# Performance work log

Measured on AMD Instinct MI355X. Metric: run time of the kernel, lower is better.

Reference implementation:

```python
import jax, jax.numpy as jnp
import numpy as np

B, C, H, W = 256, 3, 224, 224
CROP = 190


def _persp_coeffs(end):
    # torchvision _get_perspective_coeffs: solve for (a..h) with
    # (a*ex+b*ey+c)/(g*ex+h*ey+1)=sx, (d*ex+e*ey+f)/(g*ex+h*ey+1)=sy
    start = jnp.array([[0., 0.], [223., 0.], [223., 223.], [0., 223.]], jnp.float32)
    ex, ey = end[:, 0], end[:, 1]
    sx, sy = start[:, 0], start[:, 1]
    o = jnp.ones(4, jnp.float32); z = jnp.zeros(4, jnp.float32)
    r1 = jnp.stack([ex, ey, o, z, z, z, -sx * ex, -sx * ey], axis=-1)
    r2 = jnp.stack([z, z, z, ex, ey, o, -sy * ex, -sy * ey], axis=-1)
    A = jnp.concatenate([r1, r2], axis=0)  # [8,8]
    b = jnp.concatenate([sx, sy], axis=0)
    return jnp.linalg.solve(A, b)


def _bilinear(img, sx, sy):
    # img [C,H,W]; sx,sy [H,W] source index coords; zero padding outside.
    Hh, Ww = img.shape[-2], img.shape[-1]
    x0 = jnp.floor(sx); y0 = jnp.floor(sy)
    wx = sx - x0; wy = sy - y0
    x0i = x0.astype(jnp.int32); y0i = y0.astype(jnp.int32)

    def tap(yi, xi, w):
        valid = ((xi >= 0) & (xi < Ww) & (yi >= 0) & (yi < Hh)).astype(img.dtype)
        v = img[:, jnp.clip(yi, 0, Hh - 1), jnp.clip(xi, 0, Ww - 1)]
        return v * (w * valid)[None]

    return (tap(y0i, x0i, (1 - wx) * (1 - wy)) + tap(y0i, x0i + 1, wx * (1 - wy))
            + tap(y0i + 1, x0i, (1 - wx) * wy) + tap(y0i + 1, x0i + 1, wx * wy))


def _augment(x, noise, brightness, flip_mask, ep_raw, angles, crop_ij):
    Bb, Cc, Hh, Ww = x.shape
    # random hflip
    x = jnp.where(flip_mask[:, None, None, None] > 0, x[..., ::-1], x)
    # gaussian noise (std 0.625) and brightness in [0.85, 1.15]
    x = x + 0.625 * noise
    x = x * (0.85 + 0.30 * brightness)[:, None, None, None]
    # batched perspective warp (bilinear, zero fill)
    offs = jnp.array([[0., 0.], [195., 0.], [195., 195.], [0., 195.]], jnp.float32)
    end = ep_raw.astype(jnp.float32) + offs  # [B,4,2] endpoints
    coeffs = jax.vmap(_persp_coeffs)(end)    # [B,8]
    Xg, Yg = jnp.meshgrid(jnp.arange(Ww, dtype=jnp.float32) + 0.5,
                          jnp.arange(Hh, dtype=jnp.float32) + 0.5, indexing='xy')
    a, b, c, d, e, f, g, h = [coeffs[:, i][:, None, None] for i in range(8)]
    den = g * Xg + h * Yg + 1.0
    sx = (a * Xg + b * Yg + c) / den - 0.5  # half-pixel centers, align_corners=False
    sy = (d * Xg + e * Yg + f) / den - 0.5
    x = jax.vmap(_bilinear)(x, sx, sy)
    # batched rotation about image center (bilinear, zero fill)
    th = (angles.astype(jnp.float32) - 16.0) * (jnp.pi / 180.0)
    cos = jnp.cos(th)[:, None, None]; sin = jnp.sin(th)[:, None, None]
    cx = (Ww - 1) / 2.0; cy = (Hh - 1) / 2.0
    dx = (Xg - 0.5) - cx; dy = (Yg - 0.5) - cy
    rx = cos * dx + sin * dy + cx
    ry = -sin * dx + cos * dy + cy
    x = jax.vmap(_bilinear)(x, rx, ry)
    # per-sample 190x190 crop
    x = jax.vmap(lambda img, ij: jax.lax.dynamic_slice(
        img, (0, ij[0], ij[1]), (Cc, CROP, CROP)))(x, crop_ij)
    # bicubic resize back to 224x224
    x = jax.image.resize(x, (Bb, Cc, Hh, Ww), method='bicubic')
    return x


def setup_inputs() -> dict:
    key = jax.random.key(0)
    ks = jax.random.split(key, 7)
    return {
        'x': jax.random.uniform(ks[0], (B, C, H, W), dtype=jnp.float32),
        'noise': jax.random.normal(ks[1], (B, C, H, W), dtype=jnp.float32),
        'brightness': jax.random.uniform(ks[2], (B,), dtype=jnp.float32),
        'flip_mask': jax.random.randint(ks[3], (B,), 0, 2, dtype=jnp.int32),
        'ep_raw': jax.random.randint(ks[4], (B, 4, 2), 0, 29, dtype=jnp.int32),
        'angles': jax.random.randint(ks[5], (B,), 0, 33, dtype=jnp.int32),
        'crop_ij': jax.random.randint(ks[6], (B, 2), 0, 35, dtype=jnp.int32),
    }


def reference(x, noise, brightness, flip_mask, ep_raw, angles, crop_ij):
    return _augment(x, noise, brightness, flip_mask, ep_raw, angles, crop_ij)
```

## Files before the change

### kernel.cpp

```cpp
#include <hip/hip_runtime.h>
#include <math.h>

#define Bn 256
#define Cn 3
#define Hn 224
#define Wn 224
#define CROPD 190

static constexpr long long NTOT = (long long)Bn * Cn * Hn * Wn;
static constexpr int PLANE = Hn * Wn;

#define TILE 32
#define TSTR 68
#define PH 48
#define PSTR 52
#define RSTR 40

#define NWG (768 * 49)
#define CHUNK (NWG / 8)

__device__ int    g_i0[Wn];
__device__ float4 g_wt[Wn];

__device__ __forceinline__ float keys_cubic(float x) {
    if (x < 1.f) return ((1.5f * x - 2.5f) * x) * x + 1.f;
    if (x < 2.f) return ((-0.5f * x + 2.5f) * x - 4.f) * x + 2.f;
    return 0.f;
}
__device__ __forceinline__ float rflf(float v) {
    return __int_as_float(__builtin_amdgcn_readfirstlane(__float_as_int(v)));
}
__device__ __forceinline__ int rfli(int v) { return __builtin_amdgcn_readfirstlane(v); }
__device__ __forceinline__ int swz_block(int bid) {
    return (bid & 7) * CHUNK + (bid >> 3);
}

__global__ void params_kernel(const int* __restrict__ ep_raw,
                              const int* __restrict__ angles,
                              const float* __restrict__ brightness,
                              const int* __restrict__ flip_mask,
                              float* __restrict__ params) {
    int b = threadIdx.x;

    if (b < Wn) {
        float sf = ((float)b + 0.5f) * ((float)CROPD / (float)Wn) - 0.5f;
        int i0 = (int)floorf(sf);
        float w[4]; float s = 0.f;
#pragma unroll
        for (int k = 0; k < 4; k++) {
            int idx = i0 - 1 + k;
            float wk = (idx >= 0 && idx < CROPD) ? keys_cubic(fabsf(sf - (float)idx)) : 0.f;
            w[k] = wk; s += wk;
        }
        float inv = 1.f / s;
        g_i0[b] = i0;
        g_wt[b] = make_float4(w[0] * inv, w[1] * inv, w[2] * inv, w[3] * inv);
    }

    if (b >= Bn) return;

    const double offx[4] = {0.0, 195.0, 195.0, 0.0};
    const double offy[4] = {0.0, 0.0, 195.0, 195.0};
    const double sxc[4]  = {0.0, 223.0, 223.0, 0.0};
    const double syc[4]  = {0.0, 0.0, 223.0, 223.0};
    double M[8][9];
    for (int i = 0; i < 4; i++) {
        double ex = (double)ep_raw[b * 8 + i * 2 + 0] + offx[i];
        double ey = (double)ep_raw[b * 8 + i * 2 + 1] + offy[i];
        double sx = sxc[i], sy = syc[i];
        M[i][0] = ex; M[i][1] = ey; M[i][2] = 1.0;
        M[i][3] = 0.0; M[i][4] = 0.0; M[i][5] = 0.0;
        M[i][6] = -sx * ex; M[i][7] = -sx * ey; M[i][8] = sx;
        M[i + 4][0] = 0.0; M[i + 4][1] = 0.0; M[i + 4][2] = 0.0;
        M[i + 4][3] = ex; M[i + 4][4] = ey; M[i + 4][5] = 1.0;
        M[i + 4][6] = -sy * ex; M[i + 4][7] = -sy * ey; M[i + 4][8] = sy;
    }
    for (int k = 0; k < 8; k++) {
        int piv = k; double best = fabs(M[k][k]);
        for (int r = k + 1; r < 8; r++) {
            double v = fabs(M[r][k]);
            if (v > best) { best = v; piv = r; }
        }
        if (piv != k)
            for (int j = 0; j < 9; j++) { double tt = M[k][j]; M[k][j] = M[piv][j]; M[piv][j] = tt; }
        double inv = 1.0 / M[k][k];
        for (int r = k + 1; r < 8; r++) {
            double f = M[r][k] * inv;
            M[r][k] = 0.0;
            for (int j = k + 1; j < 9; j++) M[r][j] -= f * M[k][j];
        }
    }
    double sol[8];
    for (int k = 7; k >= 0; k--) {
        double s = M[k][8];
        for (int j = k + 1; j < 8; j++) s -= M[k][j] * sol[j];
        sol[k] = s / M[k][k];
    }
    float* p = params + b * 12;
    for (int j = 0; j < 8; j++) p[j] = (float)sol[j];
    double th = ((double)angles[b] - 16.0) * (M_PI / 180.0);
    p[8]  = (float)cos(th);
    p[9]  = (float)sin(th);
    p[10] = 0.85f + 0.3f * brightness[b];
    p[11] = (flip_mask[b] > 0) ? 1.0f : 0.0f;
}

__global__ void meta_kernel(const float* __restrict__ params,
                            const int* __restrict__ crop_ij,
                            int4* __restrict__ pmeta,
                            int4* __restrict__ rmeta) {
    int bt = blockIdx.x * 256 + threadIdx.x;
    int b = bt / 49, t = bt % 49;
    int ty = (t / 7) * TILE, tx = (t % 7) * TILE;
    const float* prm = params + b * 12;

    {
        float a0 = prm[0], a1 = prm[1], a2 = prm[2];
        float a3 = prm[3], a4 = prm[4], a5 = prm[5];
        float g = prm[6], h = prm[7];
        float minsx = 1e30f, maxsx = -1e30f, minsy = 1e30f, maxsy = -1e30f;
#pragma unroll
        for (int cy = 0; cy < 2; cy++) {
#pragma unroll
            for (int cxr = 0; cxr < 2; cxr++) {
                float Xg = (float)tx + (cxr ? 31.5f : 0.5f);
                float Yg = (float)ty + (cy ? 31.5f : 0.5f);
                float rden = 1.0f / (g * Xg + h * Yg + 1.0f);
                float sx = (a0 * Xg + a1 * Yg + a2) * rden - 0.5f;
                float sy = (a3 * Xg + a4 * Yg + a5) * rden - 0.5f;
                minsx = fminf(minsx, sx); maxsx = fmaxf(maxsx, sx);
                minsy = fminf(minsy, sy); maxsy = fmaxf(maxsy, sy);
            }
        }
        int x0b = min(max((int)floorf(minsx) - 1, 0), Wn - 1);
        int x1b = min(max((int)floorf(maxsx) + 2, 0), Wn - 1);
        int y0b = min(max((int)floorf(minsy) - 1, 0), Hn - 1);
        int y1b = min(max((int)floorf(maxsy) + 2, 0), Hn - 1);
        x0b &= ~3;
        int bw = x1b - x0b + 1, bh = y1b - y0b + 1;
        int inter = (minsx >= 0.5f && maxsx <= 222.0f &&
                     minsy >= 0.5f && maxsy <= 222.0f) ? 1 : 0;
        pmeta[bt] = make_int4(x0b, y0b, bw | (inter << 16), bh);
    }

    {
        float cs = prm[8], sn = prm[9];
        int ci = crop_ij[b * 2 + 0], cj = crop_ij[b * 2 + 1];
        int iymin = max(g_i0[ty] - 1, 0);
        int iymax = min(g_i0[ty + 31] + 2, CROPD - 1);
        int jmin = max(g_i0[tx] - 1, 0);
        int jmax = min(g_i0[tx + 31] + 2, CROPD - 1);
        int ry0 = iymin + ci, ry1 = iymax + ci;
        int rx0 = jmin + cj, rx1 = jmax + cj;
        const float cxc = (Wn - 1) * 0.5f;
        float minrx = 1e30f, maxrx = -1e30f, minry = 1e30f, maxry = -1e30f;
#pragma unroll
        for (int cy = 0; cy < 2; cy++) {
#pragma unroll
            for (int cxr = 0; cxr < 2; cxr++) {
                float dx = (float)(cxr ? rx1 : rx0) - cxc;
                float dy = (float)(cy ? ry1 : ry0) - cxc;
                float rx = cs * dx + sn * dy + cxc;
                float ry = -sn * dx + cs * dy + cxc;
                minrx = fminf(minrx, rx); maxrx = fmaxf(maxrx, rx);
                minry = fminf(minry, ry); maxry = fmaxf(maxry, ry);
            }
        }
        int x0b = min(max((int)floorf(minrx) - 1, 0), Wn - 1);
        int x1b = min(max((int)floorf(maxrx) + 2, 0), Wn - 1);
        int y0b = min(max((int)floorf(minry) - 1, 0), Hn - 1);
        int y1b = min(max((int)floorf(maxry) + 2, 0), Hn - 1);
        x0b &= ~3;
        int bw = x1b - x0b + 1, bh = y1b - y0b + 1;
        int inter = (minrx >= 0.5f && maxrx <= 222.0f &&
                     minry >= 0.5f && maxry <= 222.0f) ? 1 : 0;
        rmeta[bt] = make_int4(x0b, y0b, bw | (inter << 16), bh);
    }
}

__global__ __launch_bounds__(256) void persp_kernel(const float* __restrict__ xin,
                                                    const float* __restrict__ noise,
                                                    const float* __restrict__ params,
                                                    const int4* __restrict__ pmeta,
                                                    float* __restrict__ outP) {
    __shared__ __align__(16) float lds[64 * TSTR];
    int bi = swz_block(blockIdx.x);
    int p = bi / 49;
    int t = bi % 49;
    int ty = (t / 7) * TILE;
    int tx = (t % 7) * TILE;
    int b = p / Cn;
    int4 m = pmeta[b * 49 + t];
    int x0b = m.x, y0b = m.y;
    int bw = m.z & 0xffff;
    bool interior = (m.z >> 16) != 0;
    int bh = m.w;
    int y1b = y0b + bh - 1;
    bool use_lds = (bw <= 64) && (bh <= 64);

    const float* prm = params + b * 12;
    float a0 = rflf(prm[0]), a1 = rflf(prm[1]), a2 = rflf(prm[2]);
    float a3 = rflf(prm[3]), a4 = rflf(prm[4]), a5 = rflf(prm[5]);
    float g = rflf(prm[6]), h = rflf(prm[7]), bf = rflf(prm[10]);
    bool flip = rflf(prm[11]) > 0.5f;

    const size_t base = (size_t)p * PLANE;
    const float* xb = xin + base;
    const float* nb = noise + base;
    int tid = threadIdx.x;

    if (use_lds) {
        int bwq = (bw + 3) >> 2;
        int sh = (bwq <= 8) ? 3 : 4;
        int c4 = tid & ((1 << sh) - 1);
        int r0 = tid >> sh;
        int rstep = 256 >> sh;
        bool cok = c4 < bwq;
        for (int yy = y0b + r0; yy <= y1b; yy += rstep) {
            if (cok) {
                int xl = min(x0b + c4 * 4, Wn - 4);
                float4 nv = *reinterpret_cast<const float4*>(&nb[yy * Wn + xl]);
                float4 xv;
                if (flip) {
                    float4 xr = *reinterpret_cast<const float4*>(&xb[yy * Wn + (Wn - 4 - xl)]);
                    xv = make_float4(xr.w, xr.z, xr.y, xr.x);
                } else {
                    xv = *reinterpret_cast<const float4*>(&xb[yy * Wn + xl]);
                }
                float4 f = make_float4((xv.x + 0.625f * nv.x) * bf,
                                       (xv.y + 0.625f * nv.y) * bf,
                                       (xv.z + 0.625f * nv.z) * bf,
                                       (xv.w + 0.625f * nv.w) * bf);
                *reinterpret_cast<float4*>(&lds[(yy - y0b) * TSTR + (xl - x0b)]) = f;
            }
        }
        __syncthreads();
    }

    int r = tid >> 3;
    int cg = tid & 7;
    int oy = ty + r, ox0 = tx + cg * 4;
    float Yg = (float)oy + 0.5f;
    float Xg0 = (float)ox0 + 0.5f;
    float nx = a0 * Xg0 + a1 * Yg + a2;
    float ny = a3 * Xg0 + a4 * Yg + a5;
    float dn = g * Xg0 + h * Yg + 1.0f;
    float racc[4];
    if (use_lds && interior) {
#pragma unroll
        for (int o = 0; o < 4; o++) {
            float rden = __builtin_amdgcn_rcpf(dn);
            float sx = nx * rden - 0.5f;
            float sy = ny * rden - 0.5f;
            float fx0 = floorf(sx), fy0 = floorf(sy);
            float wx = sx - fx0, wy = sy - fy0;
            const float* q = &lds[((int)fy0 - y0b) * TSTR + ((int)fx0 - x0b)];
            float top = q[0] + wx * (q[1] - q[0]);
            float bot = q[TSTR] + wx * (q[TSTR + 1] - q[TSTR]);
            racc[o] = top + wy * (bot - top);
            nx += a0; ny += a3; dn += g;
        }
    } else {
#pragma unroll
        for (int o = 0; o < 4; o++) {
            float rden = __builtin_amdgcn_rcpf(dn);
            float sx = nx * rden - 0.5f;
            float sy = ny * rden - 0.5f;
            float fx0 = floorf(sx), fy0 = floorf(sy);
            float wx = sx - fx0, wy = sy - fy0;
            int x0 = (int)fx0, y0 = (int)fy0;
            float acc = 0.f;
#pragma unroll
            for (int dy = 0; dy < 2; dy++) {
                int yy = y0 + dy;
                float wyv = dy ? wy : 1.f - wy;
                bool yv = (unsigned)yy < (unsigned)Hn;
                int yc = min(max(yy, 0), Hn - 1);
#pragma unroll
                for (int dx = 0; dx < 2; dx++) {
                    int xx = x0 + dx;
                    float wxv = dx ? wx : 1.f - wx;
                    bool v = yv && ((unsigned)xx < (unsigned)Wn);
                    int xc = min(max(xx, 0), Wn - 1);
                    float wgt = v ? wxv * wyv : 0.f;
                    float val;
                    if (use_lds) {
                        val = lds[(yc - y0b) * TSTR + (xc - x0b)];
                    } else {
                        int xsrc = flip ? (Wn - 1 - xc) : xc;
                        val = (xb[yc * Wn + xsrc] + 0.625f * nb[yc * Wn + xc]) * bf;
                    }
                    acc += val * wgt;
                }
            }
            racc[o] = acc;
            nx += a0; ny += a3; dn += g;
        }
    }
    *reinterpret_cast<float4*>(outP + base + (size_t)oy * Wn + ox0) =
        make_float4(racc[0], racc[1], racc[2], racc[3]);
}

__global__ __launch_bounds__(256) void rotresize_kernel(const float* __restrict__ P,
                                                        const float* __restrict__ params,
                                                        const int* __restrict__ crop_ij,
                                                        const int4* __restrict__ rmeta,
                                                        float* __restrict__ out) {
    __shared__ __align__(16) float Plds[PH * PSTR];
    __shared__ __align__(16) float Rlds[32 * RSTR];
    __shared__ __align__(16) float Tlds[32 * RSTR];
    int bi = swz_block(blockIdx.x);
    int p = bi / 49;
    int t = bi % 49;
    int ty = (t / 7) * TILE;
    int tx = (t % 7) * TILE;
    int b = p / Cn;
    int4 m = rmeta[b * 49 + t];
    int x0b = m.x, y0b = m.y;
    int bw = m.z & 0xffff;
    bool interior = (m.z >> 16) != 0;
    int bh = m.w;
    int y1b = y0b + bh - 1;
    bool use_lds = (bw <= PH) && (bh <= PH);

    const float* prm = params + b * 12;
    float cs = rflf(prm[8]), sn = rflf(prm[9]);
    int ci = rfli(crop_ij[b * 2 + 0]);
    int cj = rfli(crop_ij[b * 2 + 1]);
    int iymin = max(g_i0[ty] - 1, 0);
    int nTy = min(g_i0[ty + 31] + 2, CROPD - 1) - iymin + 1;
    int jmin = max(g_i0[tx] - 1, 0);
    int nRx = min(g_i0[tx + 31] + 2, CROPD - 1) - jmin + 1;
    int rx0 = jmin + cj, ry0 = iymin + ci;
    const float cxc = (Wn - 1) * 0.5f;

    const float* Pb = P + (size_t)p * PLANE;
    int tid = threadIdx.x;

    if (use_lds) {
        int bwq = (bw + 3) >> 2;
        int sh = (bwq <= 8) ? 3 : 4;
        int c4 = tid & ((1 << sh) - 1);
        int r0 = tid >> sh;
        int rstep = 256 >> sh;
        bool cok = c4 < bwq;
        for (int yy = y0b + r0; yy <= y1b; yy += rstep) {
            if (cok) {
                int xl = min(x0b + c4 * 4, Wn - 4);
                float4 v = *reinterpret_cast<const float4*>(&Pb[yy * Wn + xl]);
                *reinterpret_cast<float4*>(&Plds[(yy - y0b) * PSTR + (xl - x0b)]) = v;
            }
        }
        __syncthreads();
    }

    {
        int rc = tid & 31;
        int rbase = tid >> 5;
        bool cok = rc < nRx;
        float dxc = (float)(rx0 + rc) - cxc;
        float bx = cs * dxc + cxc;
        float by = -sn * dxc + cxc;
        if (use_lds && interior) {
#pragma unroll
            for (int it = 0; it < 4; it++) {
                int rr = it * 8 + rbase;
                if (rr < nTy && cok) {
                    float dyr = (float)(ry0 + rr) - cxc;
                    float srx = bx + sn * dyr;
                    float sry = by + cs * dyr;
                    float fx0 = floorf(srx), fy0 = floorf(sry);
                    float wx = srx - fx0, wy = sry - fy0;
                    const float* q = &Plds[((int)fy0 - y0b) * PSTR + ((int)fx0 - x0b)];
                    float top = q[0] + wx * (q[1] - q[0]);
                    float bot = q[PSTR] + wx * (q[PSTR + 1] - q[PSTR]);
                    Rlds[rr * RSTR + rc] = top + wy * (bot - top);
                }
            }
        } else {
#pragma unroll
            for (int it = 0; it < 4; it++) {
                int rr = it * 8 + rbase;
                if (rr < nTy && cok) {
                    float dyr = (float)(ry0 + rr) - cxc;
                    float srx = bx + sn * dyr;
                    float sry = by + cs * dyr;
                    float fx0 = floorf(srx), fy0 = floorf(sry);
                    float wx = srx - fx0, wy = sry - fy0;
                    int x0 = (int)fx0, y0 = (int)fy0;
                    float acc = 0.f;
#pragma unroll
                    for (int ddy = 0; ddy < 2; ddy++) {
                        int yy = y0 + ddy;
                        float wyv = ddy ? wy : 1.f - wy;
                        bool yv = (unsigned)yy < (unsigned)Hn;
                        int yc = min(max(yy, 0), Hn - 1);
#pragma unroll
                        for (int ddx = 0; ddx < 2; ddx++) {
                            int xx = x0 + ddx;
                            float wxv = ddx ? wx : 1.f - wx;
                            bool v = yv && ((unsigned)xx < (unsigned)Wn);
                            int xc = min(max(xx, 0), Wn - 1);
                            float wgt = v ? wxv * wyv : 0.f;
                            float val = use_lds ? Plds[(yc - y0b) * PSTR + (xc - x0b)]
                                                : Pb[yc * Wn + xc];
                            acc += val * wgt;
                        }
                    }
                    Rlds[rr * RSTR + rc] = acc;
                }
            }
        }
    }
    __syncthreads();

    {
        int oc = tid & 31;
        int rbase = tid >> 5;
        int ox = tx + oc;
        float4 w = g_wt[ox];
        int j0 = g_i0[ox];
        int jc0 = min(max(j0 - 1, 0), CROPD - 1) - jmin;
        int jc1 = min(max(j0 + 0, 0), CROPD - 1) - jmin;
        int jc2 = min(max(j0 + 1, 0), CROPD - 1) - jmin;
        int jc3 = min(max(j0 + 2, 0), CROPD - 1) - jmin;
#pragma unroll
        for (int it = 0; it < 4; it++) {
            int rr = it * 8 + rbase;
            if (rr < nTy) {
                const float* row = &Rlds[rr * RSTR];
                Tlds[rr * RSTR + oc] = w.x * row[jc0] + w.y * row[jc1] +
                                       w.z * row[jc2] + w.w * row[jc3];
            }
        }
    }
    __syncthreads();

    {
        int r = tid >> 3, cg = tid & 7;
        int oy = ty + r, ox0 = tx + cg * 4;
        float4 w = g_wt[oy];
        int i0y = g_i0[oy];
        float wk[4] = {w.x, w.y, w.z, w.w};
        float4 acc = make_float4(0.f, 0.f, 0.f, 0.f);
#pragma unroll
        for (int k = 0; k < 4; k++) {
            int iyc = min(max(i0y - 1 + k, 0), CROPD - 1) - iymin;
            float4 v = *reinterpret_cast<const float4*>(&Tlds[iyc * RSTR + cg * 4]);
            acc.x += wk[k] * v.x;
            acc.y += wk[k] * v.y;
            acc.z += wk[k] * v.z;
            acc.w += wk[k] * v.w;
        }
        *reinterpret_cast<float4*>(out + (size_t)p * PLANE + (size_t)oy * Wn + ox0) = acc;
    }
}

extern "C" void kernel_launch(void* const* d_in, const int* in_sizes, int n_in,
                              void* d_out, int out_size, void* d_ws, size_t ws_size,
                              hipStream_t stream) {
    const float* x          = (const float*)d_in[0];
    const float* noise      = (const float*)d_in[1];
    const float* brightness = (const float*)d_in[2];
    const int*   flip_mask  = (const int*)d_in[3];
    const int*   ep_raw     = (const int*)d_in[4];
    const int*   angles     = (const int*)d_in[5];
    const int*   crop_ij    = (const int*)d_in[6];
    float* out = (float*)d_out;

    float* params = (float*)d_ws;
    int4*  pmeta  = (int4*)((char*)d_ws + 16384);
    int4*  rmeta  = (int4*)((char*)d_ws + 16384 + 200704);
    float* Pbuf   = (float*)((char*)d_ws + (1 << 20));

    params_kernel<<<1, 256, 0, stream>>>(ep_raw, angles, brightness, flip_mask, params);
    meta_kernel<<<49, 256, 0, stream>>>(params, crop_ij, pmeta, rmeta);
    persp_kernel<<<NWG, 256, 0, stream>>>(x, noise, params, pmeta, Pbuf);
    rotresize_kernel<<<NWG, 256, 0, stream>>>(Pbuf, params, crop_ij, rmeta, out);
}
```

Before: 273.6 us.

## Fuse perspective warp into rotate-resize kernel, eliminating intermediate buffer

Merges the perspective kernel and the rotate/crop/resize kernel into one. Each tile now computes, in LDS, only the perspective-warped region its rotation needs, working from a staged input footprint derived by back-projecting the rotation bounding box. This removes the full-size intermediate write and re-read in global memory, plus one launch. The cost is redundant perspective computation across neighbouring tiles' overlapping halos, more LDS per block, and a slow global fallback path that recomputes the perspective per tap.

```diff
diff --git a/kernel.cpp b/kernel.cpp
--- a/kernel.cpp
+++ b/kernel.cpp
@@ -7,12 +7,12 @@
 #define Wn 224
 #define CROPD 190
 
-static constexpr long long NTOT = (long long)Bn * Cn * Hn * Wn;
 static constexpr int PLANE = Hn * Wn;
 
 #define TILE 32
-#define TSTR 68
-#define PH 48
+#define FH 72
+#define FSTR 76
+#define PHR 48
 #define PSTR 52
 #define RSTR 40
 
@@ -107,42 +107,14 @@
 
 __global__ void meta_kernel(const float* __restrict__ params,
                             const int* __restrict__ crop_ij,
-                            int4* __restrict__ pmeta,
-                            int4* __restrict__ rmeta) {
+                            int4* __restrict__ rmeta,
+                            int4* __restrict__ smeta) {
     int bt = blockIdx.x * 256 + threadIdx.x;
     int b = bt / 49, t = bt % 49;
     int ty = (t / 7) * TILE, tx = (t % 7) * TILE;
     const float* prm = params + b * 12;
 
-    {
-        float a0 = prm[0], a1 = prm[1], a2 = prm[2];
-        float a3 = prm[3], a4 = prm[4], a5 = prm[5];
-        float g = prm[6], h = prm[7];
-        float minsx = 1e30f, maxsx = -1e30f, minsy = 1e30f, maxsy = -1e30f;
-#pragma unroll
-        for (int cy = 0; cy < 2; cy++) {
-#pragma unroll
-            for (int cxr = 0; cxr < 2; cxr++) {
-                float Xg = (float)tx + (cxr ? 31.5f : 0.5f);
-                float Yg = (float)ty + (cy ? 31.5f : 0.5f);
-                float rden = 1.0f / (g * Xg + h * Yg + 1.0f);
-                float sx = (a0 * Xg + a1 * Yg + a2) * rden - 0.5f;
-                float sy = (a3 * Xg + a4 * Yg + a5) * rden - 0.5f;
-                minsx = fminf(minsx, sx); maxsx = fmaxf(maxsx, sx);
-                minsy = fminf(minsy, sy); maxsy = fmaxf(maxsy, sy);
-            }
-        }
-        int x0b = min(max((int)floorf(minsx) - 1, 0), Wn - 1);
-        int x1b = min(max((int)floorf(maxsx) + 2, 0), Wn - 1);
-        int y0b = min(max((int)floorf(minsy) - 1, 0), Hn - 1);
-        int y1b = min(max((int)floorf(maxsy) + 2, 0), Hn - 1);
-        x0b &= ~3;
-        int bw = x1b - x0b + 1, bh = y1b - y0b + 1;
-        int inter = (minsx >= 0.5f && maxsx <= 222.0f &&
-                     minsy >= 0.5f && maxsy <= 222.0f) ? 1 : 0;
-        pmeta[bt] = make_int4(x0b, y0b, bw | (inter << 16), bh);
-    }
-
+    int x0p, y0p, bwp, bhp;
     {
         float cs = prm[8], sn = prm[9];
         int ci = crop_ij[b * 2 + 0], cj = crop_ij[b * 2 + 1];
@@ -170,55 +142,144 @@
         int x1b = min(max((int)floorf(maxrx) + 2, 0), Wn - 1);
         int y0b = min(max((int)floorf(minry) - 1, 0), Hn - 1);
         int y1b = min(max((int)floorf(maxry) + 2, 0), Hn - 1);
-        x0b &= ~3;
-        int bw = x1b - x0b + 1, bh = y1b - y0b + 1;
+        x0p = x0b; y0p = y0b;
+        bwp = x1b - x0b + 1; bhp = y1b - y0b + 1;
         int inter = (minrx >= 0.5f && maxrx <= 222.0f &&
                      minry >= 0.5f && maxry <= 222.0f) ? 1 : 0;
-        rmeta[bt] = make_int4(x0b, y0b, bw | (inter << 16), bh);
-    }
-}
-
-__global__ __launch_bounds__(256) void persp_kernel(const float* __restrict__ xin,
-                                                    const float* __restrict__ noise,
-                                                    const float* __restrict__ params,
-                                                    const int4* __restrict__ pmeta,
-                                                    float* __restrict__ outP) {
-    __shared__ __align__(16) float lds[64 * TSTR];
+        rmeta[bt] = make_int4(x0b, y0b, bwp | (inter << 16), bhp);
+    }
+
+    {
+        float a0 = prm[0], a1 = prm[1], a2 = prm[2];
+        float a3 = prm[3], a4 = prm[4], a5 = prm[5];
+        float g = prm[6], h = prm[7];
+        int x1p = x0p + bwp - 1, y1p = y0p + bhp - 1;
+        float minsx = 1e30f, maxsx = -1e30f, minsy = 1e30f, maxsy = -1e30f;
+#pragma unroll
+        for (int cy = 0; cy < 2; cy++) {
+#pragma unroll
+            for (int cxr = 0; cxr < 2; cxr++) {
+                float Xg = (float)(cxr ? x1p : x0p) + 0.5f;
+                float Yg = (float)(cy ? y1p : y0p) + 0.5f;
+                float rden = 1.0f / (g * Xg + h * Yg + 1.0f);
+                float sx = (a0 * Xg + a1 * Yg + a2) * rden - 0.5f;
+                float sy = (a3 * Xg + a4 * Yg + a5) * rden - 0.5f;
+                minsx = fminf(minsx, sx); maxsx = fmaxf(maxsx, sx);
+                minsy = fminf(minsy, sy); maxsy = fmaxf(maxsy, sy);
+            }
+        }
+        int x0s = min(max((int)floorf(minsx) - 1, 0), Wn - 1);
+        int x1s = min(max((int)floorf(maxsx) + 2, 0), Wn - 1);
+        int y0s = min(max((int)floorf(minsy) - 1, 0), Hn - 1);
+        int y1s = min(max((int)floorf(maxsy) + 2, 0), Hn - 1);
+        x0s &= ~3;
+        int bws = x1s - x0s + 1, bhs = y1s - y0s + 1;
+        int inter = (minsx >= 0.5f && maxsx <= 222.0f &&
+                     minsy >= 0.5f && maxsy <= 222.0f) ? 1 : 0;
+        smeta[bt] = make_int4(x0s, y0s, bws | (inter << 16), bhs);
+    }
+}
+
+__device__ __forceinline__ float persp_at(const float* __restrict__ xb,
+                                          const float* __restrict__ nb,
+                                          bool flip, float bf,
+                                          float a0, float a1, float a2,
+                                          float a3, float a4, float a5,
+                                          float g, float h, int ixp, int iyp) {
+    float Xg = (float)ixp + 0.5f, Yg = (float)iyp + 0.5f;
+    float rden = __builtin_amdgcn_rcpf(g * Xg + h * Yg + 1.0f);
+    float sx = (a0 * Xg + a1 * Yg + a2) * rden - 0.5f;
+    float sy = (a3 * Xg + a4 * Yg + a5) * rden - 0.5f;
+    float fx0 = floorf(sx), fy0 = floorf(sy);
+    float wx = sx - fx0, wy = sy - fy0;
+    int x0 = (int)fx0, y0 = (int)fy0;
+    float acc = 0.f;
+#pragma unroll
+    for (int dy = 0; dy < 2; dy++) {
+        int yy = y0 + dy;
+        float wyv = dy ? wy : 1.f - wy;
+        bool yv = (unsigned)yy < (unsigned)Hn;
+        int yc = min(max(yy, 0), Hn - 1);
+#pragma unroll
+        for (int dx = 0; dx < 2; dx++) {
+            int xx = x0 + dx;
+            float wxv = dx ? wx : 1.f - wx;
+            bool v = yv && ((unsigned)xx < (unsigned)Wn);
+            int xc = min(max(xx, 0), Wn - 1);
+            float wgt = v ? wxv * wyv : 0.f;
+            int xs = flip ? (Wn - 1 - xc) : xc;
+            acc += (xb[yc * Wn + xs] + 0.625f * nb[yc * Wn + xc]) * bf * wgt;
+        }
+    }
+    return acc;
+}
+
+__global__ __launch_bounds__(256) void mega_kernel(const float* __restrict__ xin,
+                                                   const float* __restrict__ noise,
+                                                   const float* __restrict__ params,
+                                                   const int* __restrict__ crop_ij,
+                                                   const int4* __restrict__ rmeta,
+                                                   const int4* __restrict__ smeta,
+                                                   float* __restrict__ out) {
+    __shared__ __align__(16) float smem[FH * FSTR + PHR * PSTR];
+    float* Flds = smem;
+    float* Plds = smem + FH * FSTR;
+    float* Rlds = smem;
+    float* Tlds = smem + 32 * RSTR;
+
     int bi = swz_block(blockIdx.x);
     int p = bi / 49;
     int t = bi % 49;
     int ty = (t / 7) * TILE;
     int tx = (t % 7) * TILE;
     int b = p / Cn;
-    int4 m = pmeta[b * 49 + t];
-    int x0b = m.x, y0b = m.y;
-    int bw = m.z & 0xffff;
-    bool interior = (m.z >> 16) != 0;
-    int bh = m.w;
-    int y1b = y0b + bh - 1;
-    bool use_lds = (bw <= 64) && (bh <= 64);
+    int tid = threadIdx.x;
+
+    int4 rm = rmeta[b * 49 + t];
+    int x0p = rm.x, y0p = rm.y;
+    int bwp = rm.z & 0xffff;
+    bool interior_r = (rm.z >> 16) != 0;
+    int bhp = rm.w;
+    int4 sm = smeta[b * 49 + t];
+    int x0s = sm.x, y0s = sm.y;
+    int bws = sm.z & 0xffff;
+    bool interior_s = (sm.z >> 16) != 0;
+    int bhs = sm.w;
+    int y1s = y0s + bhs - 1;
+    bool fitF = (bws <= FH) && (bhs <= FH);
+    bool fitP = (bwp <= PHR) && (bhp <= PHR);
+    bool fast = fitF && fitP;
 
     const float* prm = params + b * 12;
     float a0 = rflf(prm[0]), a1 = rflf(prm[1]), a2 = rflf(prm[2]);
     float a3 = rflf(prm[3]), a4 = rflf(prm[4]), a5 = rflf(prm[5]);
     float g = rflf(prm[6]), h = rflf(prm[7]), bf = rflf(prm[10]);
+    float cs = rflf(prm[8]), sn = rflf(prm[9]);
     bool flip = rflf(prm[11]) > 0.5f;
+    int ci = rfli(crop_ij[b * 2 + 0]);
+    int cj = rfli(crop_ij[b * 2 + 1]);
+
+    int iymin = max(g_i0[ty] - 1, 0);
+    int nTy = min(g_i0[ty + 31] + 2, CROPD - 1) - iymin + 1;
+    int jmin = max(g_i0[tx] - 1, 0);
+    int nRx = min(g_i0[tx + 31] + 2, CROPD - 1) - jmin + 1;
+    int rx0 = jmin + cj, ry0 = iymin + ci;
+    const float cxc = (Wn - 1) * 0.5f;
 
     const size_t base = (size_t)p * PLANE;
     const float* xb = xin + base;
     const float* nb = noise + base;
-    int tid = threadIdx.x;
-
-    if (use_lds) {
-        int bwq = (bw + 3) >> 2;
-        int sh = (bwq <= 8) ? 3 : 4;
+
+    if (fast) {
+        int bwq = (bws + 3) >> 2;
+        int sh = (bwq <= 8) ? 3 : ((bwq <= 16) ? 4 : 5);
         int c4 = tid & ((1 << sh) - 1);
         int r0 = tid >> sh;
         int rstep = 256 >> sh;
         bool cok = c4 < bwq;
-        for (int yy = y0b + r0; yy <= y1b; yy += rstep) {
+        for (int yy = y0s + r0; yy <= y1s; yy += rstep) {
             if (cok) {
-                int xl = min(x0b + c4 * 4, Wn - 4);
+                int xl = min(x0s + c4 * 4, Wn - 4);
                 float4 nv = *reinterpret_cast<const float4*>(&nb[yy * Wn + xl]);
                 float4 xv;
                 if (flip) {
@@ -231,128 +292,80 @@
                                        (xv.y + 0.625f * nv.y) * bf,
                                        (xv.z + 0.625f * nv.z) * bf,
                                        (xv.w + 0.625f * nv.w) * bf);
-                *reinterpret_cast<float4*>(&lds[(yy - y0b) * TSTR + (xl - x0b)]) = f;
-            }
-        }
-        __syncthreads();
-    }
-
-    int r = tid >> 3;
-    int cg = tid & 7;
-    int oy = ty + r, ox0 = tx + cg * 4;
-    float Yg = (float)oy + 0.5f;
-    float Xg0 = (float)ox0 + 0.5f;
-    float nx = a0 * Xg0 + a1 * Yg + a2;
-    float ny = a3 * Xg0 + a4 * Yg + a5;
-    float dn = g * Xg0 + h * Yg + 1.0f;
-    float racc[4];
-    if (use_lds && interior) {
-#pragma unroll
-        for (int o = 0; o < 4; o++) {
-            float rden = __builtin_amdgcn_rcpf(dn);
-            float sx = nx * rden - 0.5f;
-            float sy = ny * rden - 0.5f;
-            float fx0 = floorf(sx), fy0 = floorf(sy);
-            float wx = sx - fx0, wy = sy - fy0;
-            const float* q = &lds[((int)fy0 - y0b) * TSTR + ((int)fx0 - x0b)];
-            float top = q[0] + wx * (q[1] - q[0]);
-            float bot = q[TSTR] + wx * (q[TSTR + 1] - q[TSTR]);
-            racc[o] = top + wy * (bot - top);
-            nx += a0; ny += a3; dn += g;
-        }
-    } else {
-#pragma unroll
-        for (int o = 0; o < 4; o++) {
-            float rden = __builtin_amdgcn_rcpf(dn);
-            float sx = nx * rden - 0.5f;
-            float sy = ny * rden - 0.5f;
-            float fx0 = floorf(sx), fy0 = floorf(sy);
-            float wx = sx - fx0, wy = sy - fy0;
-            int x0 = (int)fx0, y0 = (int)fy0;
-            float acc = 0.f;
-#pragma unroll
-            for (int dy = 0; dy < 2; dy++) {
-                int yy = y0 + dy;
-                float wyv = dy ? wy : 1.f - wy;
-                bool yv = (unsigned)yy < (unsigned)Hn;
-                int yc = min(max(yy, 0), Hn - 1);
-#pragma unroll
-                for (int dx = 0; dx < 2; dx++) {
-                    int xx = x0 + dx;
-                    float wxv = dx ? wx : 1.f - wx;
-                    bool v = yv && ((unsigned)xx < (unsigned)Wn);
-                    int xc = min(max(xx, 0), Wn - 1);
-                    float wgt = v ? wxv * wyv : 0.f;
-                    float val;
-                    if (use_lds) {
-                        val = lds[(yc - y0b) * TSTR + (xc - x0b)];
-                    } else {
-                        int xsrc = flip ? (Wn - 1 - xc) : xc;
-                        val = (xb[yc * Wn + xsrc] + 0.625f * nb[yc * Wn + xc]) * bf;
+                *reinterpret_cast<float4*>(&Flds[(yy - y0s) * FSTR + (xl - x0s)]) = f;
+            }
+        }
+    }
+    __syncthreads();
+
+    if (fast) {
+        int bwpq = (bwp + 3) >> 2;
+        int c4 = tid & 15;
+        int r0 = tid >> 4;
+        bool cok = c4 < bwpq;
+        int x1p = x0p + bwp - 1;
+        if (interior_s) {
+            for (int pr = r0; pr < bhp; pr += 16) {
+                if (!cok) continue;
+                float Yg = (float)(y0p + pr) + 0.5f;
+                float pv[4];
+#pragma unroll
+                for (int j = 0; j < 4; j++) {
+                    int px = min(x0p + c4 * 4 + j, x1p);
+                    float Xg = (float)px + 0.5f;
+                    float rden = __builtin_amdgcn_rcpf(g * Xg + h * Yg + 1.0f);
+                    float sx = (a0 * Xg + a1 * Yg + a2) * rden - 0.5f;
+                    float sy = (a3 * Xg + a4 * Yg + a5) * rden - 0.5f;
+                    float fx0 = floorf(sx), fy0 = floorf(sy);
+                    float wx = sx - fx0, wy = sy - fy0;
+                    const float* q = &Flds[((int)fy0 - y0s) * FSTR + ((int)fx0 - x0s)];
+                    float top = q[0] + wx * (q[1] - q[0]);
+                    float bot = q[FSTR] + wx * (q[FSTR + 1] - q[FSTR]);
+                    pv[j] = top + wy * (bot - top);
+                }
+                *reinterpret_cast<float4*>(&Plds[pr * PSTR + c4 * 4]) =
+                    make_float4(pv[0], pv[1], pv[2], pv[3]);
+            }
+        } else {
+            for (int pr = r0; pr < bhp; pr += 16) {
+                if (!cok) continue;
+                float Yg = (float)(y0p + pr) + 0.5f;
+                float pv[4];
+#pragma unroll
+                for (int j = 0; j < 4; j++) {
+                    int px = min(x0p + c4 * 4 + j, x1p);
+                    float Xg = (float)px + 0.5f;
+                    float rden = __builtin_amdgcn_rcpf(g * Xg + h * Yg + 1.0f);
+                    float sx = (a0 * Xg + a1 * Yg + a2) * rden - 0.5f;
+                    float sy = (a3 * Xg + a4 * Yg + a5) * rden - 0.5f;
+                    float fx0 = floorf(sx), fy0 = floorf(sy);
+                    float wx = sx - fx0, wy = sy - fy0;
+                    int x0 = (int)fx0, y0 = (int)fy0;
+                    float acc = 0.f;
+#pragma unroll
+                    for (int dy = 0; dy < 2; dy++) {
+                        int yy = y0 + dy;
+                        float wyv = dy ? wy : 1.f - wy;
+                        bool yv = (unsigned)yy < (unsigned)Hn;
+                        int yc = min(max(yy, 0), Hn - 1);
+#pragma unroll
+                        for (int dx = 0; dx < 2; dx++) {
+                            int xx = x0 + dx;
+                            float wxv = dx ? wx : 1.f - wx;
+                            bool v = yv && ((unsigned)xx < (unsigned)Wn);
+                            int xc = min(max(xx, 0), Wn - 1);
+                            float wgt = v ? wxv * wyv : 0.f;
+                            acc += Flds[(yc - y0s) * FSTR + (xc - x0s)] * wgt;
+                        }
                     }
-                    acc += val * wgt;
+                    pv[j] = acc;
                 }
-            }
-            racc[o] = acc;
-            nx += a0; ny += a3; dn += g;
-        }
-    }
-    *reinterpret_cast<float4*>(outP + base + (size_t)oy * Wn + ox0) =
-        make_float4(racc[0], racc[1], racc[2], racc[3]);
-}
-
-__global__ __launch_bounds__(256) void rotresize_kernel(const float* __restrict__ P,
-                                                        const float* __restrict__ params,
-                                                        const int* __restrict__ crop_ij,
-                                                        const int4* __restrict__ rmeta,
-                                                        float* __restrict__ out) {
-    __shared__ __align__(16) float Plds[PH * PSTR];
-    __shared__ __align__(16) float Rlds[32 * RSTR];
-    __shared__ __align__(16) float Tlds[32 * RSTR];
-    int bi = swz_block(blockIdx.x);
-    int p = bi / 49;
-    int t = bi % 49;
-    int ty = (t / 7) * TILE;
-    int tx = (t % 7) * TILE;
-    int b = p / Cn;
-    int4 m = rmeta[b * 49 + t];
-    int x0b = m.x, y0b = m.y;
-    int bw = m.z & 0xffff;
-    bool interior = (m.z >> 16) != 0;
-    int bh = m.w;
-    int y1b = y0b + bh - 1;
-    bool use_lds = (bw <= PH) && (bh <= PH);
-
-    const float* prm = params + b * 12;
-    float cs = rflf(prm[8]), sn = rflf(prm[9]);
-    int ci = rfli(crop_ij[b * 2 + 0]);
-    int cj = rfli(crop_ij[b * 2 + 1]);
-    int iymin = max(g_i0[ty] - 1, 0);
-    int nTy = min(g_i0[ty + 31] + 2, CROPD - 1) - iymin + 1;
-    int jmin = max(g_i0[tx] - 1, 0);
-    int nRx = min(g_i0[tx + 31] + 2, CROPD - 1) - jmin + 1;
-    int rx0 = jmin + cj, ry0 = iymin + ci;
-    const float cxc = (Wn - 1) * 0.5f;
-
-    const float* Pb = P + (size_t)p * PLANE;
-    int tid = threadIdx.x;
-
-    if (use_lds) {
-        int bwq = (bw + 3) >> 2;
-        int sh = (bwq <= 8) ? 3 : 4;
-        int c4 = tid & ((1 << sh) - 1);
-        int r0 = tid >> sh;
-        int rstep = 256 >> sh;
-        bool cok = c4 < bwq;
-        for (int yy = y0b + r0; yy <= y1b; yy += rstep) {
-            if (cok) {
-                int xl = min(x0b + c4 * 4, Wn - 4);
-                float4 v = *reinterpret_cast<const float4*>(&Pb[yy * Wn + xl]);
-                *reinterpret_cast<float4*>(&Plds[(yy - y0b) * PSTR + (xl - x0b)]) = v;
-            }
-        }
-        __syncthreads();
-    }
+                *reinterpret_cast<float4*>(&Plds[pr * PSTR + c4 * 4]) =
+                    make_float4(pv[0], pv[1], pv[2], pv[3]);
+            }
+        }
+    }
+    __syncthreads();
 
     {
         int rc = tid & 31;
@@ -361,7 +374,7 @@
         float dxc = (float)(rx0 + rc) - cxc;
         float bx = cs * dxc + cxc;
         float by = -sn * dxc + cxc;
-        if (use_lds && interior) {
+        if (fast && interior_r) {
 #pragma unroll
             for (int it = 0; it < 4; it++) {
                 int rr = it * 8 + rbase;
@@ -371,13 +384,13 @@
                     float sry = by + cs * dyr;
                     float fx0 = floorf(srx), fy0 = floorf(sry);
                     float wx = srx - fx0, wy = sry - fy0;
-                    const float* q = &Plds[((int)fy0 - y0b) * PSTR + ((int)fx0 - x0b)];
+                    const float* q = &Plds[((int)fy0 - y0p) * PSTR + ((int)fx0 - x0p)];
                     float top = q[0] + wx * (q[1] - q[0]);
                     float bot = q[PSTR] + wx * (q[PSTR + 1] - q[PSTR]);
                     Rlds[rr * RSTR + rc] = top + wy * (bot - top);
                 }
             }
-        } else {
+        } else if (fast) {
 #pragma unroll
             for (int it = 0; it < 4; it++) {
                 int rr = it * 8 + rbase;
@@ -402,9 +415,40 @@
                             bool v = yv && ((unsigned)xx < (unsigned)Wn);
                             int xc = min(max(xx, 0), Wn - 1);
                             float wgt = v ? wxv * wyv : 0.f;
-                            float val = use_lds ? Plds[(yc - y0b) * PSTR + (xc - x0b)]
-                                                : Pb[yc * Wn + xc];
-                            acc += val * wgt;
+                            acc += Plds[(yc - y0p) * PSTR + (xc - x0p)] * wgt;
+                        }
+                    }
+                    Rlds[rr * RSTR + rc] = acc;
+                }
+            }
+        } else {
+#pragma unroll
+            for (int it = 0; it < 4; it++) {
+                int rr = it * 8 + rbase;
+                if (rr < nTy && cok) {
+                    float dyr = (float)(ry0 + rr) - cxc;
+                    float srx = bx + sn * dyr;
+                    float sry = by + cs * dyr;
+                    float fx0 = floorf(srx), fy0 = floorf(sry);
+                    float wx = srx - fx0, wy = sry - fy0;
+                    int x0 = (int)fx0, y0 = (int)fy0;
+                    float acc = 0.f;
+#pragma unroll
+                    for (int ddy = 0; ddy < 2; ddy++) {
+                        int yy = y0 + ddy;
+                        float wyv = ddy ? wy : 1.f - wy;
+                        bool yv = (unsigned)yy < (unsigned)Hn;
+                        int yc = min(max(yy, 0), Hn - 1);
+#pragma unroll
+                        for (int ddx = 0; ddx < 2; ddx++) {
+                            int xx = x0 + ddx;
+                            float wxv = ddx ? wx : 1.f - wx;
+                            bool v = yv && ((unsigned)xx < (unsigned)Wn);
+                            int xc = min(max(xx, 0), Wn - 1);
+                            float wgt = v ? wxv * wyv : 0.f;
+                            if (wgt != 0.f)
+                                acc += persp_at(xb, nb, flip, bf, a0, a1, a2,
+                                                a3, a4, a5, g, h, xc, yc) * wgt;
                         }
                     }
                     Rlds[rr * RSTR + rc] = acc;
@@ -452,7 +496,7 @@
             acc.z += wk[k] * v.z;
             acc.w += wk[k] * v.w;
         }
-        *reinterpret_cast<float4*>(out + (size_t)p * PLANE + (size_t)oy * Wn + ox0) = acc;
+        *reinterpret_cast<float4*>(out + base + (size_t)oy * Wn + ox0) = acc;
     }
 }
 
@@ -469,12 +513,10 @@
     float* out = (float*)d_out;
 
     float* params = (float*)d_ws;
-    int4*  pmeta  = (int4*)((char*)d_ws + 16384);
-    int4*  rmeta  = (int4*)((char*)d_ws + 16384 + 200704);
-    float* Pbuf   = (float*)((char*)d_ws + (1 << 20));
+    int4*  rmeta  = (int4*)((char*)d_ws + 16384);
+    int4*  smeta  = (int4*)((char*)d_ws + 16384 + 200704);
 
     params_kernel<<<1, 256, 0, stream>>>(ep_raw, angles, brightness, flip_mask, params);
-    meta_kernel<<<49, 256, 0, stream>>>(params, crop_ij, pmeta, rmeta);
-    persp_kernel<<<NWG, 256, 0, stream>>>(x, noise, params, pmeta, Pbuf);
-    rotresize_kernel<<<NWG, 256, 0, stream>>>(Pbuf, params, crop_ij, rmeta, out);
-}
+    meta_kernel<<<49, 256, 0, stream>>>(params, crop_ij, rmeta, smeta);
+    mega_kernel<<<NWG, 256, 0, stream>>>(x, noise, params, crop_ij, rmeta, smeta, out);
+}
```

Result: no change. 270.9 us (-1.0%).
